# Kernel optimization log

Measured on AMD Instinct MI355X. Metric: run time of the kernel, lower is better.

The kernel has to match this reference:

```python
import jax, jax.numpy as jnp
import numpy as np

B, D, L = 64, 1024, 2048  # batch, init dim, source length; context feature dim = D//2


def setup_inputs() -> dict:
    key = jax.random.key(0)
    k1, k2, k3, k4 = jax.random.split(key, 4)
    inp = jax.random.normal(k1, (B, D), dtype=jnp.float32)
    context = jax.random.normal(k2, (B, L, D // 2), dtype=jnp.float32)
    # torch Linear weights: [out_features, in_features]
    W_in = jax.random.normal(k3, (D, D), dtype=jnp.float32) * (1.0 / np.sqrt(D))
    W_out = jax.random.normal(k4, (D, 2 * D), dtype=jnp.float32) * (1.0 / np.sqrt(2 * D))
    return {"input": inp, "context": context, "W_in": W_in, "W_out": W_out}


def reference(input, context, W_in, W_out):
    Bv, Dv = input.shape
    # linear_in(input).view(B, D//2, 2): two query vectors of size D//2 per batch
    targetT = (input @ W_in.T).reshape(Bv, Dv // 2, 2)           # [B, D/2, 2]
    attn = jnp.einsum('bld,bdk->bkl', context, targetT)          # [B, 2, L]
    attn = jax.nn.softmax(attn, axis=-1)                         # softmax over sourceL
    weighted = jnp.einsum('bkl,bld->bkd', attn, context)         # [B, 2, D/2]
    weightedContext = weighted.reshape(Bv, Dv)                   # [B, D]
    combined = jnp.concatenate([weightedContext, input], axis=1) # [B, 2D]
    contextOutput = jnp.tanh(combined @ W_out.T)                 # [B, D]
    return contextOutput, attn[:, 0, :], attn[:, 1, :]
```

## Files before the change

kernel.cpp:

```cpp
#include <hip/hip_runtime.h>
#include <cmath>

#define NB 64
#define ND 1024
#define DH 512
#define NL 2048
#define NCHUNK 16
#define RPB 128
#define RPW 32
#define REC 520

__global__ __launch_bounds__(256) void k_gemm(const float* __restrict__ A,
                                              const float* __restrict__ W,
                                              float* __restrict__ out,
                                              int K, int do_tanh) {
  __shared__ float As[64][65];
  __shared__ float Ws[4][65];
  const int t = threadIdx.x;
  const int jt = blockIdx.x * 4;
  const int b = t & 63, jl = t >> 6;
  float acc = 0.f;
  for (int m0 = 0; m0 < K; m0 += 64) {
#pragma unroll
    for (int i = 0; i < 4; i++) {
      int f = t + i * 256;
      int r = f >> 4, c = (f & 15) * 4;
      const float4 v = *(const float4*)(A + (size_t)r * K + m0 + c);
      As[r][c] = v.x; As[r][c + 1] = v.y; As[r][c + 2] = v.z; As[r][c + 3] = v.w;
    }
    if (t < 64) {
      int r = t >> 4, c = (t & 15) * 4;
      const float4 v = *(const float4*)(W + (size_t)(jt + r) * K + m0 + c);
      Ws[r][c] = v.x; Ws[r][c + 1] = v.y; Ws[r][c + 2] = v.z; Ws[r][c + 3] = v.w;
    }
    __syncthreads();
#pragma unroll
    for (int mm = 0; mm < 64; mm++) acc += As[b][mm] * Ws[jl][mm];
    __syncthreads();
  }
  out[(size_t)b * ND + jt + jl] = do_tanh ? tanhf(acc) : acc;
}

__global__ __launch_bounds__(256, 4) void k2_attn(const float* __restrict__ ctx,
                                                  const float* __restrict__ tgt,
                                                  float* __restrict__ sc0,
                                                  float* __restrict__ sc1,
                                                  float* __restrict__ part) {
  const int chunk = blockIdx.x, b = blockIdx.y;
  const int wave = threadIdx.x >> 6, lane = threadIdx.x & 63;
  const float* crow = ctx + ((size_t)b * NL + chunk * RPB + wave * RPW) * DH + lane * 8;

  float t0[8], t1[8];
  {
    const float* tp = tgt + b * ND + lane * 16;
#pragma unroll
    for (int j = 0; j < 4; j++) {
      float4 v = *(const float4*)(tp + j * 4);
      t0[2 * j] = v.x; t1[2 * j] = v.y; t0[2 * j + 1] = v.z; t1[2 * j + 1] = v.w;
    }
  }

  float m0 = -INFINITY, l0 = 0.f, m1 = -INFINITY, l1 = 0.f;
  float a0[8], a1[8];
#pragma unroll
  for (int j = 0; j < 8; j++) { a0[j] = 0.f; a1[j] = 0.f; }
  float sv0 = 0.f, sv1 = 0.f;

  float4 pa = *(const float4*)(crow);
  float4 pb = *(const float4*)(crow + 4);
#pragma unroll 2
  for (int i = 0; i < RPW; i++) {
    float c[8] = {pa.x, pa.y, pa.z, pa.w, pb.x, pb.y, pb.z, pb.w};
    if (i + 1 < RPW) {
      pa = *(const float4*)(crow + (size_t)(i + 1) * DH);
      pb = *(const float4*)(crow + (size_t)(i + 1) * DH + 4);
    }
    float s0 = 0.f, s1 = 0.f;
#pragma unroll
    for (int j = 0; j < 8; j++) { s0 += c[j] * t0[j]; s1 += c[j] * t1[j]; }
#pragma unroll
    for (int off = 32; off > 0; off >>= 1) {
      s0 += __shfl_xor(s0, off);
      s1 += __shfl_xor(s1, off);
    }
    if (lane == i) { sv0 = s0; sv1 = s1; }
    if (s0 > m0) {
      float al = __expf(m0 - s0);
      m0 = s0; l0 *= al;
#pragma unroll
      for (int j = 0; j < 8; j++) a0[j] *= al;
    }
    {
      float p = __expf(s0 - m0);
      l0 += p;
#pragma unroll
      for (int j = 0; j < 8; j++) a0[j] += p * c[j];
    }
    if (s1 > m1) {
      float al = __expf(m1 - s1);
      m1 = s1; l1 *= al;
#pragma unroll
      for (int j = 0; j < 8; j++) a1[j] *= al;
    }
    {
      float p = __expf(s1 - m1);
      l1 += p;
#pragma unroll
      for (int j = 0; j < 8; j++) a1[j] += p * c[j];
    }
  }

  const int rowbase = b * NL + chunk * RPB + wave * RPW;
  if (lane < RPW) { sc0[rowbase + lane] = sv0; sc1[rowbase + lane] = sv1; }

  __shared__ float accS[4][1024];
  __shared__ float mlS[4][4];
#pragma unroll
  for (int j = 0; j < 8; j++) {
    accS[wave][lane * 8 + j] = a0[j];
    accS[wave][512 + lane * 8 + j] = a1[j];
  }
  if (lane == 0) { mlS[wave][0] = m0; mlS[wave][1] = l0; mlS[wave][2] = m1; mlS[wave][3] = l1; }
  __syncthreads();

  const int t = threadIdx.x;
  const int k = (t * 4) >> 9;
  const int d = (t * 4) & 511;
  float M = fmaxf(fmaxf(mlS[0][2 * k], mlS[1][2 * k]), fmaxf(mlS[2][2 * k], mlS[3][2 * k]));
  float Lk = 0.f;
  float v0 = 0.f, v1 = 0.f, v2 = 0.f, v3 = 0.f;
#pragma unroll
  for (int w = 0; w < 4; w++) {
    float e = __expf(mlS[w][2 * k] - M);
    Lk += mlS[w][2 * k + 1] * e;
    const float* ap = &accS[w][k * 512 + d];
    v0 += ap[0] * e; v1 += ap[1] * e; v2 += ap[2] * e; v3 += ap[3] * e;
  }
  float* rec = part + ((size_t)(b * NCHUNK + chunk) * 2 + k) * REC;
  if ((t & 127) == 0) { rec[0] = M; rec[1] = Lk; }
  rec[4 + d] = v0; rec[5 + d] = v1; rec[6 + d] = v2; rec[7 + d] = v3;
}

__global__ __launch_bounds__(256) void k3_combine(const float* __restrict__ part,
                                                  const float* __restrict__ inp,
                                                  float* __restrict__ combined,
                                                  float* __restrict__ sc0,
                                                  float* __restrict__ sc1) {
  const int b = blockIdx.x;
  const int t = threadIdx.x;
  __shared__ float MM[2], LL[2];
  if (t < 2) {
    const int k = t;
    float Mk = -INFINITY;
    for (int c = 0; c < NCHUNK; c++)
      Mk = fmaxf(Mk, part[((size_t)(b * NCHUNK + c) * 2 + k) * REC]);
    float Lk = 0.f;
    for (int c = 0; c < NCHUNK; c++) {
      const float* rec = part + ((size_t)(b * NCHUNK + c) * 2 + k) * REC;
      Lk += rec[1] * __expf(rec[0] - Mk);
    }
    MM[k] = Mk; LL[k] = Lk;
  }
  __syncthreads();

  const int k = (t * 4) >> 9, d = (t * 4) & 511;
  float v0 = 0.f, v1 = 0.f, v2 = 0.f, v3 = 0.f;
  for (int c = 0; c < NCHUNK; c++) {
    const float* rec = part + ((size_t)(b * NCHUNK + c) * 2 + k) * REC;
    float e = __expf(rec[0] - MM[k]);
    v0 += rec[4 + d] * e; v1 += rec[5 + d] * e; v2 += rec[6 + d] * e; v3 += rec[7 + d] * e;
  }
  const float inv = 1.f / LL[k];
  float* cp = combined + (size_t)b * 2048 + k * 512 + d;
  cp[0] = v0 * inv; cp[1] = v1 * inv; cp[2] = v2 * inv; cp[3] = v3 * inv;

  const float4 iv = *(const float4*)(inp + (size_t)b * ND + t * 4);
  *(float4*)(combined + (size_t)b * 2048 + 1024 + t * 4) = iv;

  const float M0 = MM[0], i0 = 1.f / LL[0];
  const float M1 = MM[1], i1 = 1.f / LL[1];
#pragma unroll
  for (int r = 0; r < 8; r++) {
    const int idx = b * NL + t * 8 + r;
    sc0[idx] = __expf(sc0[idx] - M0) * i0;
    sc1[idx] = __expf(sc1[idx] - M1) * i1;
  }
}

extern "C" void kernel_launch(void* const* d_in, const int* in_sizes, int n_in,
                              void* d_out, int out_size, void* d_ws, size_t ws_size,
                              hipStream_t stream) {
  const float* input   = (const float*)d_in[0];
  const float* context = (const float*)d_in[1];
  const float* W_in    = (const float*)d_in[2];
  const float* W_out   = (const float*)d_in[3];

  float* out   = (float*)d_out;
  float* attn0 = out + NB * ND;
  float* attn1 = attn0 + NB * NL;

  float* ws       = (float*)d_ws;
  float* target   = ws;
  float* combined = ws + NB * ND;
  float* part     = ws + NB * ND + NB * 2048;

  k_gemm<<<dim3(ND / 4), dim3(256), 0, stream>>>(input, W_in, target, ND, 0);
  k2_attn<<<dim3(NCHUNK, NB), dim3(256), 0, stream>>>(context, target, attn0, attn1, part);
  k3_combine<<<dim3(NB), dim3(256), 0, stream>>>(part, input, combined, attn0, attn1);
  k_gemm<<<dim3(ND / 4), dim3(256), 0, stream>>>(combined, W_out, out, 2 * ND, 1);
}
```

Measured before the change: 451.5 us.

## Replace GEMM with transposed-activation scalar-weight kernel and block attention softmax by four rows

Both linear layers now transpose the 64-row activation into a K-by-64 layout first. A new GEMM kernel then has each lane own one batch row and each wave compute two output columns, with weights read as wave-uniform scalars. The attention kernel handles four context rows per step: it batches the shuffle reductions and does one online-softmax rescale per group instead of per row, and prefetches the next four rows. The occupancy hint drops from 4 to 2 blocks per SM. This adds two transpose launches and more registers per thread.

```diff
diff --git a/kernel.cpp b/kernel.cpp
--- a/kernel.cpp
+++ b/kernel.cpp
@@ -10,38 +10,50 @@
 #define RPW 32
 #define REC 520
 
-__global__ __launch_bounds__(256) void k_gemm(const float* __restrict__ A,
-                                              const float* __restrict__ W,
-                                              float* __restrict__ out,
-                                              int K, int do_tanh) {
-  __shared__ float As[64][65];
-  __shared__ float Ws[4][65];
+__global__ __launch_bounds__(256) void k_transpose(const float* __restrict__ in,
+                                                   float* __restrict__ out, int K) {
+  __shared__ float tile[64][65];
+  const int m0 = blockIdx.x * 64;
   const int t = threadIdx.x;
-  const int jt = blockIdx.x * 4;
-  const int b = t & 63, jl = t >> 6;
-  float acc = 0.f;
-  for (int m0 = 0; m0 < K; m0 += 64) {
-#pragma unroll
-    for (int i = 0; i < 4; i++) {
-      int f = t + i * 256;
-      int r = f >> 4, c = (f & 15) * 4;
-      const float4 v = *(const float4*)(A + (size_t)r * K + m0 + c);
-      As[r][c] = v.x; As[r][c + 1] = v.y; As[r][c + 2] = v.z; As[r][c + 3] = v.w;
-    }
-    if (t < 64) {
-      int r = t >> 4, c = (t & 15) * 4;
-      const float4 v = *(const float4*)(W + (size_t)(jt + r) * K + m0 + c);
-      Ws[r][c] = v.x; Ws[r][c + 1] = v.y; Ws[r][c + 2] = v.z; Ws[r][c + 3] = v.w;
-    }
-    __syncthreads();
-#pragma unroll
-    for (int mm = 0; mm < 64; mm++) acc += As[b][mm] * Ws[jl][mm];
-    __syncthreads();
-  }
-  out[(size_t)b * ND + jt + jl] = do_tanh ? tanhf(acc) : acc;
-}
-
-__global__ __launch_bounds__(256, 4) void k2_attn(const float* __restrict__ ctx,
+  const int lm = t & 63;
+  const int q = t >> 6;
+#pragma unroll
+  for (int i = 0; i < 16; i++) {
+    int b = q * 16 + i;
+    tile[b][lm] = in[(size_t)b * K + m0 + lm];
+  }
+  __syncthreads();
+#pragma unroll
+  for (int i = 0; i < 16; i++) {
+    int m = q * 16 + i;
+    out[(size_t)(m0 + m) * 64 + lm] = tile[lm][m];
+  }
+}
+
+template <int KK, int ACT>
+__global__ __launch_bounds__(256) void k_gemmT(const float* __restrict__ AT,
+                                               const float* __restrict__ W,
+                                               float* __restrict__ out) {
+  const int lane = threadIdx.x & 63;
+  const int wv = threadIdx.x >> 6;
+  const int j0 = __builtin_amdgcn_readfirstlane((int)(blockIdx.x * 8 + wv * 2));
+  const float* w0 = W + (size_t)j0 * KK;
+  const float* w1 = w0 + KK;
+  float acc0 = 0.f, acc1 = 0.f;
+  for (int m = 0; m < KK; m += 8) {
+#pragma unroll
+    for (int u = 0; u < 8; u++) {
+      float a = AT[(size_t)(m + u) * 64 + lane];
+      acc0 = fmaf(a, w0[m + u], acc0);
+      acc1 = fmaf(a, w1[m + u], acc1);
+    }
+  }
+  float* o = out + (size_t)lane * ND + j0;
+  if (ACT) { o[0] = tanhf(acc0); o[1] = tanhf(acc1); }
+  else     { o[0] = acc0;        o[1] = acc1; }
+}
+
+__global__ __launch_bounds__(256, 2) void k2_attn(const float* __restrict__ ctx,
                                                   const float* __restrict__ tgt,
                                                   float* __restrict__ sc0,
                                                   float* __restrict__ sc1,
@@ -66,48 +78,70 @@
   for (int j = 0; j < 8; j++) { a0[j] = 0.f; a1[j] = 0.f; }
   float sv0 = 0.f, sv1 = 0.f;
 
-  float4 pa = *(const float4*)(crow);
-  float4 pb = *(const float4*)(crow + 4);
-#pragma unroll 2
-  for (int i = 0; i < RPW; i++) {
-    float c[8] = {pa.x, pa.y, pa.z, pa.w, pb.x, pb.y, pb.z, pb.w};
-    if (i + 1 < RPW) {
-      pa = *(const float4*)(crow + (size_t)(i + 1) * DH);
-      pb = *(const float4*)(crow + (size_t)(i + 1) * DH + 4);
-    }
-    float s0 = 0.f, s1 = 0.f;
-#pragma unroll
-    for (int j = 0; j < 8; j++) { s0 += c[j] * t0[j]; s1 += c[j] * t1[j]; }
-#pragma unroll
-    for (int off = 32; off > 0; off >>= 1) {
-      s0 += __shfl_xor(s0, off);
-      s1 += __shfl_xor(s1, off);
-    }
-    if (lane == i) { sv0 = s0; sv1 = s1; }
-    if (s0 > m0) {
-      float al = __expf(m0 - s0);
-      m0 = s0; l0 *= al;
-#pragma unroll
-      for (int j = 0; j < 8; j++) a0[j] *= al;
-    }
+  float4 cur[8], nxt[8];
+#pragma unroll
+  for (int r = 0; r < 4; r++) {
+    cur[2 * r]     = *(const float4*)(crow + (size_t)r * DH);
+    cur[2 * r + 1] = *(const float4*)(crow + (size_t)r * DH + 4);
+  }
+
+#pragma unroll
+  for (int ib = 0; ib < 8; ib++) {
+    if (ib < 7) {
+#pragma unroll
+      for (int r = 0; r < 4; r++) {
+        nxt[2 * r]     = *(const float4*)(crow + (size_t)((ib + 1) * 4 + r) * DH);
+        nxt[2 * r + 1] = *(const float4*)(crow + (size_t)((ib + 1) * 4 + r) * DH + 4);
+      }
+    }
+    const float* C = (const float*)cur;
+
+    float s0[4], s1[4];
+#pragma unroll
+    for (int r = 0; r < 4; r++) {
+      float x0 = 0.f, x1 = 0.f;
+#pragma unroll
+      for (int j = 0; j < 8; j++) { x0 += C[r * 8 + j] * t0[j]; x1 += C[r * 8 + j] * t1[j]; }
+      s0[r] = x0; s1[r] = x1;
+    }
+#pragma unroll
+    for (int off = 32; off; off >>= 1) {
+#pragma unroll
+      for (int r = 0; r < 4; r++) {
+        s0[r] += __shfl_xor(s0[r], off);
+        s1[r] += __shfl_xor(s1[r], off);
+      }
+    }
+#pragma unroll
+    for (int r = 0; r < 4; r++)
+      if (lane == ib * 4 + r) { sv0 = s0[r]; sv1 = s1[r]; }
+
     {
-      float p = __expf(s0 - m0);
-      l0 += p;
-#pragma unroll
-      for (int j = 0; j < 8; j++) a0[j] += p * c[j];
-    }
-    if (s1 > m1) {
-      float al = __expf(m1 - s1);
-      m1 = s1; l1 *= al;
-#pragma unroll
-      for (int j = 0; j < 8; j++) a1[j] *= al;
+      float M = fmaxf(fmaxf(s0[0], s0[1]), fmaxf(s0[2], s0[3]));
+      float mn = fmaxf(m0, M);
+      float al = __expf(m0 - mn);
+      float p0 = __expf(s0[0] - mn), p1 = __expf(s0[1] - mn);
+      float p2 = __expf(s0[2] - mn), p3 = __expf(s0[3] - mn);
+      l0 = l0 * al + ((p0 + p1) + (p2 + p3));
+      m0 = mn;
+#pragma unroll
+      for (int j = 0; j < 8; j++)
+        a0[j] = a0[j] * al + p0 * C[j] + p1 * C[8 + j] + p2 * C[16 + j] + p3 * C[24 + j];
     }
     {
-      float p = __expf(s1 - m1);
-      l1 += p;
-#pragma unroll
-      for (int j = 0; j < 8; j++) a1[j] += p * c[j];
-    }
+      float M = fmaxf(fmaxf(s1[0], s1[1]), fmaxf(s1[2], s1[3]));
+      float mn = fmaxf(m1, M);
+      float al = __expf(m1 - mn);
+      float p0 = __expf(s1[0] - mn), p1 = __expf(s1[1] - mn);
+      float p2 = __expf(s1[2] - mn), p3 = __expf(s1[3] - mn);
+      l1 = l1 * al + ((p0 + p1) + (p2 + p3));
+      m1 = mn;
+#pragma unroll
+      for (int j = 0; j < 8; j++)
+        a1[j] = a1[j] * al + p0 * C[j] + p1 * C[8 + j] + p2 * C[16 + j] + p3 * C[24 + j];
+    }
+#pragma unroll
+    for (int i = 0; i < 8; i++) cur[i] = nxt[i];
   }
 
   const int rowbase = b * NL + chunk * RPB + wave * RPW;
@@ -201,11 +235,15 @@
 
   float* ws       = (float*)d_ws;
   float* target   = ws;
-  float* combined = ws + NB * ND;
-  float* part     = ws + NB * ND + NB * 2048;
-
-  k_gemm<<<dim3(ND / 4), dim3(256), 0, stream>>>(input, W_in, target, ND, 0);
+  float* combined = target + NB * ND;
+  float* AT1      = combined + NB * 2048;
+  float* ATc      = AT1 + ND * 64;
+  float* part     = ATc + 2 * ND * 64;
+
+  k_transpose<<<dim3(ND / 64), dim3(256), 0, stream>>>(input, AT1, ND);
+  k_gemmT<ND, 0><<<dim3(ND / 8), dim3(256), 0, stream>>>(AT1, W_in, target);
   k2_attn<<<dim3(NCHUNK, NB), dim3(256), 0, stream>>>(context, target, attn0, attn1, part);
   k3_combine<<<dim3(NB), dim3(256), 0, stream>>>(part, input, combined, attn0, attn1);
-  k_gemm<<<dim3(ND / 4), dim3(256), 0, stream>>>(combined, W_out, out, 2 * ND, 1);
-}
+  k_transpose<<<dim3(2 * ND / 64), dim3(256), 0, stream>>>(combined, ATc, 2 * ND);
+  k_gemmT<2 * ND, 1><<<dim3(ND / 8), dim3(256), 0, stream>>>(ATc, W_out, out);
+}
```

After: 574.9 us. +27.3%, slower.
